# Kernel tuning notes

Hardware: AMD Instinct MI355X
Metric: run time of the kernel (lower is better)

## Reference

```python
import jax, jax.numpy as jnp
import numpy as np

B = 128
N_ATOMS = 4096
NB, NA, NT = 4095, 4094, 4093
MAX_LEN = 5 * NT  # 20465, longest packed column (torsions)
EPS = 1e-8


def setup_inputs() -> dict:
    key = jax.random.key(0)
    ks = jax.random.split(key, 24)
    feats = jnp.zeros((B, MAX_LEN, 9), jnp.float32)
    # col 0: atom type ids
    atoms = jax.random.randint(ks[0], (B, N_ATOMS), 0, 6)
    # col 5: coords, flattened (N_ATOMS, 3)
    coords = jax.random.normal(ks[1], (B, N_ATOMS, 3), jnp.float32) * 5.0
    # col 6: bonds (i, j, type)
    bonds = jnp.stack([
        jax.random.randint(ks[2], (B, NB), 0, N_ATOMS),
        jax.random.randint(ks[3], (B, NB), 0, N_ATOMS),
        jax.random.randint(ks[4], (B, NB), 0, 15)], axis=-1)
    # col 7: angles (i, j, k, type)
    angles = jnp.stack([
        jax.random.randint(ks[5], (B, NA), 0, N_ATOMS),
        jax.random.randint(ks[6], (B, NA), 0, N_ATOMS),
        jax.random.randint(ks[7], (B, NA), 0, N_ATOMS),
        jax.random.randint(ks[8], (B, NA), 0, 13)], axis=-1)
    # col 8: torsions (i, j, k, l, type)
    tors = jnp.stack([
        jax.random.randint(ks[9], (B, NT), 0, N_ATOMS),
        jax.random.randint(ks[10], (B, NT), 0, N_ATOMS),
        jax.random.randint(ks[11], (B, NT), 0, N_ATOMS),
        jax.random.randint(ks[12], (B, NT), 0, N_ATOMS),
        jax.random.randint(ks[13], (B, NT), 0, 25)], axis=-1)
    feats = feats.at[:, :N_ATOMS, 0].set(atoms.astype(jnp.float32))
    feats = feats.at[:, :3 * N_ATOMS, 5].set(coords.reshape(B, -1))
    feats = feats.at[:, :3 * NB, 6].set(bonds.reshape(B, -1).astype(jnp.float32))
    feats = feats.at[:, :4 * NA, 7].set(angles.reshape(B, -1).astype(jnp.float32))
    feats = feats.at[:, :5 * NT, 8].set(tors.reshape(B, -1).astype(jnp.float32))
    lengths = jnp.tile(jnp.array(
        [[N_ATOMS, 0, 0, 0, 0, 3 * N_ATOMS, 3 * NB, 4 * NA, 5 * NT]],
        jnp.int32), (B, 1))
    bond_type = jnp.stack([jnp.ones(15), jax.random.uniform(ks[14], (15,), minval=1.0, maxval=2.0)], -1).astype(jnp.float32)
    angle_type = jnp.stack([jnp.ones(13), jax.random.uniform(ks[15], (13,), minval=1.0, maxval=3.0)], -1).astype(jnp.float32)
    tor_type = jnp.stack([jnp.ones(25), jax.random.uniform(ks[16], (25,), minval=0.0, maxval=3.14)], -1).astype(jnp.float32)
    multiplicity = jax.random.randint(ks[17], (25,), 1, 4)
    opt_pars = jax.random.uniform(ks[18], (47,), minval=0.5, maxval=1.5).astype(jnp.float32)
    return {"features": feats, "lengths": lengths, "bond_type": bond_type,
            "angle_type": angle_type, "tor_type": tor_type,
            "multiplicity": multiplicity, "opt_pars": opt_pars}


def _sample_energy(f, bond_type, angle_type, tor_type, multiplicity, opt_pars):
    coords = f[:3 * N_ATOMS, 5].reshape(-1, 3)                      # [N,3]
    bonds = f[:3 * NB, 6].astype(jnp.int32).reshape(-1, 3)          # [NB,3]
    angles = f[:4 * NA, 7].astype(jnp.int32).reshape(-1, 4)         # [NA,4]
    tors = f[:5 * NT, 8].astype(jnp.int32).reshape(-1, 5)           # [NT,5]

    # bonds: harmonic k*(r - r0)^2
    d = coords[bonds[:, 0]] - coords[bonds[:, 1]]
    r = jnp.sqrt(jnp.sum(d * d, -1) + EPS)
    pb = bond_type[bonds[:, 2]]
    e_bond = opt_pars[0] * jnp.sum(pb[:, 0] * (r - pb[:, 1]) ** 2)

    # angles: harmonic k*(theta - theta0)^2
    v1 = coords[angles[:, 0]] - coords[angles[:, 1]]
    v2 = coords[angles[:, 2]] - coords[angles[:, 1]]
    cosang = jnp.sum(v1 * v2, -1) / (
        jnp.sqrt(jnp.sum(v1 * v1, -1) + EPS) * jnp.sqrt(jnp.sum(v2 * v2, -1) + EPS))
    theta = jnp.arccos(jnp.clip(cosang, -1.0 + 1e-6, 1.0 - 1e-6))
    pa = angle_type[angles[:, 3]]
    e_ang = opt_pars[1] * jnp.sum(pa[:, 0] * (theta - pa[:, 1]) ** 2)

    # torsions: periodic k*(1 + cos(n*phi - delta))
    ci, cj, ck, cl = (coords[tors[:, m]] for m in range(4))
    b1, b2, b3 = cj - ci, ck - cj, cl - ck
    n1 = jnp.cross(b1, b2)
    n2 = jnp.cross(b2, b3)
    b2n = b2 / jnp.sqrt(jnp.sum(b2 * b2, -1, keepdims=True) + EPS)
    m1 = jnp.cross(n1, b2n)
    phi = jnp.arctan2(jnp.sum(m1 * n2, -1), jnp.sum(n1 * n2, -1))
    pt = tor_type[tors[:, 4]]
    n_mult = multiplicity[tors[:, 4]].astype(jnp.float32)
    e_tor = opt_pars[2] * jnp.sum(pt[:, 0] * (1.0 + jnp.cos(n_mult * phi - pt[:, 1])))

    return jnp.stack([e_bond, e_ang, e_tor])


def reference(features, lengths, bond_type, angle_type, tor_type, multiplicity, opt_pars):
    # lengths are uniform across batch (constants above); vmap over batch dim
    return jax.vmap(_sample_energy, in_axes=(0, None, None, None, None, None))(
        features, bond_type, angle_type, tor_type, multiplicity, opt_pars)
```

## Files before the change

kernel.cpp:

```cpp
#include <hip/hip_runtime.h>
#include <math.h>

#define BATCH    128
#define N_ATOMS  4096
#define NB       4095
#define NA       4094
#define NT       4093
#define FSTRIDE  184185
#define ROWS     20465
#define CROWS    12288
#define BROWS    12285
#define AROWS    16376
#define EPSV     1e-8f
#define THREADS  1024
#define WAVES    16
#define TPR      120

typedef float float4a __attribute__((ext_vector_type(4), aligned(4)));

__global__ __launch_bounds__(THREADS, 1) void
local_energy_v11(const float* __restrict__ F,
                 const float* __restrict__ bond_type,
                 const float* __restrict__ angle_type,
                 const float* __restrict__ tor_type,
                 const int*   __restrict__ multiplicity,
                 const float* __restrict__ opt_pars,
                 float*       __restrict__ out)
{
    __shared__ float          scc[CROWS];
    __shared__ unsigned short sbB[BROWS + 1];
    __shared__ unsigned short sbA[AROWS];
    __shared__ unsigned short sbT[ROWS + 1];
    __shared__ float sbt[30], sat[26], stt[50], smu[25];
    __shared__ float sred[WAVES * 2];

    const int b   = blockIdx.x;
    const int x   = b & 7;
    const int g   = b >> 3;
    const int s   = (g & 15) * 8 + x;
    const int p   = g >> 4;
    const int tid = threadIdx.x;
    const int w   = tid >> 6;
    const int l   = tid & 63;
    const size_t sbase = (size_t)s * FSTRIDE;

    if (tid < 30)                      sbt[tid]       = bond_type[tid];
    else if (tid >= 32 && tid < 58)    sat[tid - 32]  = angle_type[tid - 32];
    else if (tid >= 64 && tid < 114)   stt[tid - 64]  = tor_type[tid - 64];
    else if (tid >= 128 && tid < 153)  smu[tid - 128] = (float)multiplicity[tid - 128];

    const int tmax = p ? 137 : 171;
    for (int t = w; t < tmax; t += WAVES) {
        const int R0 = TPR * t + 2 * l;
        const int R1 = R0 + 1;
        float4a v0, v1;
        const bool ok0 = (R0 < ROWS);
        const bool ok1 = (R1 < ROWS);
        if (ok0) v0 = *(const float4a*)(F + sbase + (size_t)9 * R0 + 5);
        if (ok1) v1 = *(const float4a*)(F + sbase + (size_t)9 * R1 + 5);

        if (R1 < CROWS) {
            float2 c2; c2.x = v0.x; c2.y = v1.x;
            *(float2*)(scc + R0) = c2;
        }
        if (p) {
            if (R1 < BROWS) {
                unsigned pk = (unsigned)(unsigned short)(int)v0.y
                            | ((unsigned)(unsigned short)(int)v1.y << 16);
                *(unsigned*)(sbB + R0) = pk;
            } else if (R0 < BROWS) {
                sbB[R0] = (unsigned short)(int)v0.y;
            }
            if (R1 < AROWS) {
                unsigned pk = (unsigned)(unsigned short)(int)v0.z
                            | ((unsigned)(unsigned short)(int)v1.z << 16);
                *(unsigned*)(sbA + R0) = pk;
            }
        } else {
            if (ok1) {
                unsigned pk = (unsigned)(unsigned short)(int)v0.w
                            | ((unsigned)(unsigned short)(int)v1.w << 16);
                *(unsigned*)(sbT + R0) = pk;
            } else if (ok0) {
                sbT[R0] = (unsigned short)(int)v0.w;
            }
        }
    }
    __syncthreads();

    float eA = 0.f, eB = 0.f;
    if (p) {
        for (int i = tid; i < NB; i += THREADS) {
            const int a0 = sbB[3 * i + 0];
            const int a1 = sbB[3 * i + 1];
            const int bt = sbB[3 * i + 2];
            const float dx = scc[3 * a0 + 0] - scc[3 * a1 + 0];
            const float dy = scc[3 * a0 + 1] - scc[3 * a1 + 1];
            const float dz = scc[3 * a0 + 2] - scc[3 * a1 + 2];
            const float r  = sqrtf(dx * dx + dy * dy + dz * dz + EPSV);
            const float t0 = r - sbt[bt * 2 + 1];
            eA += sbt[bt * 2 + 0] * t0 * t0;
        }
        for (int i = tid; i < NA; i += THREADS) {
            const int a0 = sbA[4 * i + 0];
            const int a1 = sbA[4 * i + 1];
            const int a2 = sbA[4 * i + 2];
            const int at = sbA[4 * i + 3];
            const float v1x = scc[3 * a0 + 0] - scc[3 * a1 + 0];
            const float v1y = scc[3 * a0 + 1] - scc[3 * a1 + 1];
            const float v1z = scc[3 * a0 + 2] - scc[3 * a1 + 2];
            const float v2x = scc[3 * a2 + 0] - scc[3 * a1 + 0];
            const float v2y = scc[3 * a2 + 1] - scc[3 * a1 + 1];
            const float v2z = scc[3 * a2 + 2] - scc[3 * a1 + 2];
            const float d12 = v1x * v2x + v1y * v2y + v1z * v2z;
            const float n1  = sqrtf(v1x * v1x + v1y * v1y + v1z * v1z + EPSV);
            const float n2  = sqrtf(v2x * v2x + v2y * v2y + v2z * v2z + EPSV);
            float cosang = d12 / (n1 * n2);
            cosang = fminf(fmaxf(cosang, -1.0f + 1e-6f), 1.0f - 1e-6f);
            const float t0 = acosf(cosang) - sat[at * 2 + 1];
            eB += sat[at * 2 + 0] * t0 * t0;
        }
    } else {
        for (int i = tid; i < NT; i += THREADS) {
            const int ai = sbT[5 * i + 0];
            const int aj = sbT[5 * i + 1];
            const int ak = sbT[5 * i + 2];
            const int al = sbT[5 * i + 3];
            const int tt = sbT[5 * i + 4];
            const float b1x = scc[3*aj+0] - scc[3*ai+0];
            const float b1y = scc[3*aj+1] - scc[3*ai+1];
            const float b1z = scc[3*aj+2] - scc[3*ai+2];
            const float b2x = scc[3*ak+0] - scc[3*aj+0];
            const float b2y = scc[3*ak+1] - scc[3*aj+1];
            const float b2z = scc[3*ak+2] - scc[3*aj+2];
            const float b3x = scc[3*al+0] - scc[3*ak+0];
            const float b3y = scc[3*al+1] - scc[3*ak+1];
            const float b3z = scc[3*al+2] - scc[3*ak+2];
            const float n1x = b1y*b2z - b1z*b2y;
            const float n1y = b1z*b2x - b1x*b2z;
            const float n1z = b1x*b2y - b1y*b2x;
            const float n2x = b2y*b3z - b2z*b3y;
            const float n2y = b2z*b3x - b2x*b3z;
            const float n2z = b2x*b3y - b2y*b3x;
            const float inv = 1.0f / sqrtf(b2x*b2x + b2y*b2y + b2z*b2z + EPSV);
            const float bnx = b2x * inv, bny = b2y * inv, bnz = b2z * inv;
            const float m1x = n1y*bnz - n1z*bny;
            const float m1y = n1z*bnx - n1x*bnz;
            const float m1z = n1x*bny - n1y*bnx;
            const float phi = atan2f(m1x*n2x + m1y*n2y + m1z*n2z,
                                     n1x*n2x + n1y*n2y + n1z*n2z);
            eA += stt[tt * 2 + 0] * (1.0f + cosf(smu[tt] * phi - stt[tt * 2 + 1]));
        }
    }

    for (int off = 32; off > 0; off >>= 1) {
        eA += __shfl_down(eA, off);
        eB += __shfl_down(eB, off);
    }
    if (l == 0) {
        sred[w * 2 + 0] = eA;
        sred[w * 2 + 1] = eB;
    }
    __syncthreads();
    if (tid == 0) {
        float rA = 0.f, rB = 0.f;
        for (int i = 0; i < WAVES; ++i) { rA += sred[i * 2]; rB += sred[i * 2 + 1]; }
        if (p) {
            out[s * 3 + 0] = opt_pars[0] * rA;
            out[s * 3 + 1] = opt_pars[1] * rB;
        } else {
            out[s * 3 + 2] = opt_pars[2] * rA;
        }
    }
}

extern "C" void kernel_launch(void* const* d_in, const int* in_sizes, int n_in,
                              void* d_out, int out_size, void* d_ws, size_t ws_size,
                              hipStream_t stream) {
    const float* F            = (const float*)d_in[0];
    const float* bond_type    = (const float*)d_in[2];
    const float* angle_type   = (const float*)d_in[3];
    const float* tor_type     = (const float*)d_in[4];
    const int*   multiplicity = (const int*)  d_in[5];
    const float* opt_pars     = (const float*)d_in[6];
    float* out = (float*)d_out;

    local_energy_v11<<<dim3(BATCH * 2), dim3(THREADS), 0, stream>>>(
        F, bond_type, angle_type, tor_type, multiplicity, opt_pars, out);
}
```

Measured before the change: 155.8 us.

## Split feature extraction into separate wide-grid kernel writing compact workspace arrays

Adds a 2048-block extraction kernel that reads the strided feature rows once and writes compact coordinate and index arrays to a global workspace. The energy kernel then loads only the coordinates into shared memory and reads index arrays directly from global memory, with angle indices fetched as a single ushort4 load. The aim is more parallelism for the strided, bandwidth-bound gather and less shared-memory staging per block. It costs a second launch, an extra write and re-read pass through global memory, and index loads that are no longer coalesced in the energy loops.

```diff
diff --git a/kernel.cpp b/kernel.cpp
--- a/kernel.cpp
+++ b/kernel.cpp
@@ -12,25 +12,60 @@
 #define BROWS    12285
 #define AROWS    16376
 #define EPSV     1e-8f
-#define THREADS  1024
 #define WAVES    16
-#define TPR      120
+
+#define WS_CW_B  0
+#define WS_BW_B  6291456
+#define WS_AW_B  9437184
+#define WS_TW_B  13631488
 
 typedef float float4a __attribute__((ext_vector_type(4), aligned(4)));
 
+__global__ __launch_bounds__(256) void
+extract_k(const float* __restrict__ F, float* __restrict__ ws)
+{
+    const int b     = blockIdx.x;
+    const int x     = b & 7;
+    const int g     = b >> 3;
+    const int s     = (g & 15) * 8 + x;
+    const int slice = g >> 4;
+    const size_t sbase = (size_t)s * FSTRIDE;
+
+    float*          __restrict__ cw = (float*)((char*)ws + WS_CW_B) + (size_t)s * 12288;
+    unsigned short* __restrict__ bw = (unsigned short*)((char*)ws + WS_BW_B) + (size_t)s * 12288;
+    unsigned short* __restrict__ aw = (unsigned short*)((char*)ws + WS_AW_B) + (size_t)s * 16384;
+    unsigned short* __restrict__ tw = (unsigned short*)((char*)ws + WS_TW_B) + (size_t)s * 20472;
+
+    const int lo = slice * 1280;
+    int  r[5]; bool ok[5]; float4a v[5];
+    #pragma unroll
+    for (int k = 0; k < 5; ++k) {
+        r[k]  = lo + (int)threadIdx.x + 256 * k;
+        ok[k] = (r[k] < ROWS);
+        if (ok[k]) v[k] = *(const float4a*)(F + sbase + (size_t)9 * r[k] + 5);
+    }
+    #pragma unroll
+    for (int k = 0; k < 5; ++k) {
+        if (!ok[k]) continue;
+        const int R = r[k];
+        if (R < CROWS) cw[R] = v[k].x;
+        if (R < BROWS) bw[R] = (unsigned short)(int)v[k].y;
+        if (R < AROWS) aw[R] = (unsigned short)(int)v[k].z;
+        tw[R] = (unsigned short)(int)v[k].w;
+    }
+}
+
+#define THREADS 1024
 __global__ __launch_bounds__(THREADS, 1) void
-local_energy_v11(const float* __restrict__ F,
-                 const float* __restrict__ bond_type,
-                 const float* __restrict__ angle_type,
-                 const float* __restrict__ tor_type,
-                 const int*   __restrict__ multiplicity,
-                 const float* __restrict__ opt_pars,
-                 float*       __restrict__ out)
+energy_k(const float* __restrict__ ws,
+         const float* __restrict__ bond_type,
+         const float* __restrict__ angle_type,
+         const float* __restrict__ tor_type,
+         const int*   __restrict__ multiplicity,
+         const float* __restrict__ opt_pars,
+         float*       __restrict__ out)
 {
-    __shared__ float          scc[CROWS];
-    __shared__ unsigned short sbB[BROWS + 1];
-    __shared__ unsigned short sbA[AROWS];
-    __shared__ unsigned short sbT[ROWS + 1];
+    __shared__ float scc[CROWS];
     __shared__ float sbt[30], sat[26], stt[50], smu[25];
     __shared__ float sred[WAVES * 2];
 
@@ -42,70 +77,41 @@
     const int tid = threadIdx.x;
     const int w   = tid >> 6;
     const int l   = tid & 63;
-    const size_t sbase = (size_t)s * FSTRIDE;
 
     if (tid < 30)                      sbt[tid]       = bond_type[tid];
     else if (tid >= 32 && tid < 58)    sat[tid - 32]  = angle_type[tid - 32];
     else if (tid >= 64 && tid < 114)   stt[tid - 64]  = tor_type[tid - 64];
     else if (tid >= 128 && tid < 153)  smu[tid - 128] = (float)multiplicity[tid - 128];
 
-    const int tmax = p ? 137 : 171;
-    for (int t = w; t < tmax; t += WAVES) {
-        const int R0 = TPR * t + 2 * l;
-        const int R1 = R0 + 1;
-        float4a v0, v1;
-        const bool ok0 = (R0 < ROWS);
-        const bool ok1 = (R1 < ROWS);
-        if (ok0) v0 = *(const float4a*)(F + sbase + (size_t)9 * R0 + 5);
-        if (ok1) v1 = *(const float4a*)(F + sbase + (size_t)9 * R1 + 5);
-
-        if (R1 < CROWS) {
-            float2 c2; c2.x = v0.x; c2.y = v1.x;
-            *(float2*)(scc + R0) = c2;
-        }
-        if (p) {
-            if (R1 < BROWS) {
-                unsigned pk = (unsigned)(unsigned short)(int)v0.y
-                            | ((unsigned)(unsigned short)(int)v1.y << 16);
-                *(unsigned*)(sbB + R0) = pk;
-            } else if (R0 < BROWS) {
-                sbB[R0] = (unsigned short)(int)v0.y;
-            }
-            if (R1 < AROWS) {
-                unsigned pk = (unsigned)(unsigned short)(int)v0.z
-                            | ((unsigned)(unsigned short)(int)v1.z << 16);
-                *(unsigned*)(sbA + R0) = pk;
-            }
-        } else {
-            if (ok1) {
-                unsigned pk = (unsigned)(unsigned short)(int)v0.w
-                            | ((unsigned)(unsigned short)(int)v1.w << 16);
-                *(unsigned*)(sbT + R0) = pk;
-            } else if (ok0) {
-                sbT[R0] = (unsigned short)(int)v0.w;
-            }
-        }
+    {
+        const float4* __restrict__ c4 =
+            (const float4*)((const char*)ws + WS_CW_B + (size_t)s * 12288 * 4);
+        #pragma unroll
+        for (int i = 0; i < 3; ++i)
+            ((float4*)scc)[tid + 1024 * i] = c4[tid + 1024 * i];
     }
     __syncthreads();
 
     float eA = 0.f, eB = 0.f;
     if (p) {
+        const unsigned short* __restrict__ bwp =
+            (const unsigned short*)((const char*)ws + WS_BW_B) + (size_t)s * 12288;
         for (int i = tid; i < NB; i += THREADS) {
-            const int a0 = sbB[3 * i + 0];
-            const int a1 = sbB[3 * i + 1];
-            const int bt = sbB[3 * i + 2];
+            const int a0 = bwp[3 * i + 0];
+            const int a1 = bwp[3 * i + 1];
+            const int bt = bwp[3 * i + 2];
             const float dx = scc[3 * a0 + 0] - scc[3 * a1 + 0];
             const float dy = scc[3 * a0 + 1] - scc[3 * a1 + 1];
             const float dz = scc[3 * a0 + 2] - scc[3 * a1 + 2];
-            const float r  = sqrtf(dx * dx + dy * dy + dz * dz + EPSV);
-            const float t0 = r - sbt[bt * 2 + 1];
+            const float rr = sqrtf(dx * dx + dy * dy + dz * dz + EPSV);
+            const float t0 = rr - sbt[bt * 2 + 1];
             eA += sbt[bt * 2 + 0] * t0 * t0;
         }
+        const ushort4* __restrict__ awp =
+            (const ushort4*)((const char*)ws + WS_AW_B + (size_t)s * 16384 * 2);
         for (int i = tid; i < NA; i += THREADS) {
-            const int a0 = sbA[4 * i + 0];
-            const int a1 = sbA[4 * i + 1];
-            const int a2 = sbA[4 * i + 2];
-            const int at = sbA[4 * i + 3];
+            const ushort4 u = awp[i];
+            const int a0 = u.x, a1 = u.y, a2 = u.z, at = u.w;
             const float v1x = scc[3 * a0 + 0] - scc[3 * a1 + 0];
             const float v1y = scc[3 * a0 + 1] - scc[3 * a1 + 1];
             const float v1z = scc[3 * a0 + 2] - scc[3 * a1 + 2];
@@ -121,12 +127,14 @@
             eB += sat[at * 2 + 0] * t0 * t0;
         }
     } else {
+        const unsigned short* __restrict__ twp =
+            (const unsigned short*)((const char*)ws + WS_TW_B) + (size_t)s * 20472;
         for (int i = tid; i < NT; i += THREADS) {
-            const int ai = sbT[5 * i + 0];
-            const int aj = sbT[5 * i + 1];
-            const int ak = sbT[5 * i + 2];
-            const int al = sbT[5 * i + 3];
-            const int tt = sbT[5 * i + 4];
+            const int ai = twp[5 * i + 0];
+            const int aj = twp[5 * i + 1];
+            const int ak = twp[5 * i + 2];
+            const int al = twp[5 * i + 3];
+            const int tt = twp[5 * i + 4];
             const float b1x = scc[3*aj+0] - scc[3*ai+0];
             const float b1y = scc[3*aj+1] - scc[3*ai+1];
             const float b1z = scc[3*aj+2] - scc[3*ai+2];
@@ -157,10 +165,7 @@
         eA += __shfl_down(eA, off);
         eB += __shfl_down(eB, off);
     }
-    if (l == 0) {
-        sred[w * 2 + 0] = eA;
-        sred[w * 2 + 1] = eB;
-    }
+    if (l == 0) { sred[w * 2 + 0] = eA; sred[w * 2 + 1] = eB; }
     __syncthreads();
     if (tid == 0) {
         float rA = 0.f, rB = 0.f;
@@ -184,7 +189,9 @@
     const int*   multiplicity = (const int*)  d_in[5];
     const float* opt_pars     = (const float*)d_in[6];
     float* out = (float*)d_out;
+    float* ws  = (float*)d_ws;
 
-    local_energy_v11<<<dim3(BATCH * 2), dim3(THREADS), 0, stream>>>(
-        F, bond_type, angle_type, tor_type, multiplicity, opt_pars, out);
+    extract_k<<<dim3(2048), dim3(256), 0, stream>>>(F, ws);
+    energy_k<<<dim3(256), dim3(THREADS), 0, stream>>>(
+        ws, bond_type, angle_type, tor_type, multiplicity, opt_pars, out);
 }
```

After: 165.3 us. 6.1% more time.

## Merge bond/angle and torsion blocks into one block per sample

Applied to the files above, without the earlier changes.

Replaces the two-blocks-per-sample split, where one block handled bonds and angles and another handled torsions, with a single block per sample. The single block stages coordinates and all index columns into shared memory once, then computes all three energies. This removes the duplicated coordinate load and halves the grid. In exchange, fewer blocks are launched than there are compute units, and each block does roughly twice the serial work.

```diff
diff --git a/kernel.cpp b/kernel.cpp
--- a/kernel.cpp
+++ b/kernel.cpp
@@ -15,11 +15,12 @@
 #define THREADS  1024
 #define WAVES    16
 #define TPR      120
+#define NTIL     171
 
 typedef float float4a __attribute__((ext_vector_type(4), aligned(4)));
 
 __global__ __launch_bounds__(THREADS, 1) void
-local_energy_v11(const float* __restrict__ F,
+local_energy_v13(const float* __restrict__ F,
                  const float* __restrict__ bond_type,
                  const float* __restrict__ angle_type,
                  const float* __restrict__ tor_type,
@@ -32,13 +33,9 @@
     __shared__ unsigned short sbA[AROWS];
     __shared__ unsigned short sbT[ROWS + 1];
     __shared__ float sbt[30], sat[26], stt[50], smu[25];
-    __shared__ float sred[WAVES * 2];
+    __shared__ float sred[WAVES * 3];
 
-    const int b   = blockIdx.x;
-    const int x   = b & 7;
-    const int g   = b >> 3;
-    const int s   = (g & 15) * 8 + x;
-    const int p   = g >> 4;
+    const int s   = blockIdx.x;
     const int tid = threadIdx.x;
     const int w   = tid >> 6;
     const int l   = tid & 63;
@@ -49,8 +46,7 @@
     else if (tid >= 64 && tid < 114)   stt[tid - 64]  = tor_type[tid - 64];
     else if (tid >= 128 && tid < 153)  smu[tid - 128] = (float)multiplicity[tid - 128];
 
-    const int tmax = p ? 137 : 171;
-    for (int t = w; t < tmax; t += WAVES) {
+    for (int t = w; t < NTIL; t += WAVES) {
         const int R0 = TPR * t + 2 * l;
         const int R1 = R0 + 1;
         float4a v0, v1;
@@ -63,114 +59,112 @@
             float2 c2; c2.x = v0.x; c2.y = v1.x;
             *(float2*)(scc + R0) = c2;
         }
-        if (p) {
-            if (R1 < BROWS) {
-                unsigned pk = (unsigned)(unsigned short)(int)v0.y
-                            | ((unsigned)(unsigned short)(int)v1.y << 16);
-                *(unsigned*)(sbB + R0) = pk;
-            } else if (R0 < BROWS) {
-                sbB[R0] = (unsigned short)(int)v0.y;
-            }
-            if (R1 < AROWS) {
-                unsigned pk = (unsigned)(unsigned short)(int)v0.z
-                            | ((unsigned)(unsigned short)(int)v1.z << 16);
-                *(unsigned*)(sbA + R0) = pk;
-            }
-        } else {
-            if (ok1) {
-                unsigned pk = (unsigned)(unsigned short)(int)v0.w
-                            | ((unsigned)(unsigned short)(int)v1.w << 16);
-                *(unsigned*)(sbT + R0) = pk;
-            } else if (ok0) {
-                sbT[R0] = (unsigned short)(int)v0.w;
-            }
+        if (R1 < BROWS) {
+            unsigned pk = (unsigned)(unsigned short)(int)v0.y
+                        | ((unsigned)(unsigned short)(int)v1.y << 16);
+            *(unsigned*)(sbB + R0) = pk;
+        } else if (R0 < BROWS) {
+            sbB[R0] = (unsigned short)(int)v0.y;
+        }
+        if (R1 < AROWS) {
+            unsigned pk = (unsigned)(unsigned short)(int)v0.z
+                        | ((unsigned)(unsigned short)(int)v1.z << 16);
+            *(unsigned*)(sbA + R0) = pk;
+        }
+        if (ok1) {
+            unsigned pk = (unsigned)(unsigned short)(int)v0.w
+                        | ((unsigned)(unsigned short)(int)v1.w << 16);
+            *(unsigned*)(sbT + R0) = pk;
+        } else if (ok0) {
+            sbT[R0] = (unsigned short)(int)v0.w;
         }
     }
     __syncthreads();
 
-    float eA = 0.f, eB = 0.f;
-    if (p) {
-        for (int i = tid; i < NB; i += THREADS) {
-            const int a0 = sbB[3 * i + 0];
-            const int a1 = sbB[3 * i + 1];
-            const int bt = sbB[3 * i + 2];
-            const float dx = scc[3 * a0 + 0] - scc[3 * a1 + 0];
-            const float dy = scc[3 * a0 + 1] - scc[3 * a1 + 1];
-            const float dz = scc[3 * a0 + 2] - scc[3 * a1 + 2];
-            const float r  = sqrtf(dx * dx + dy * dy + dz * dz + EPSV);
-            const float t0 = r - sbt[bt * 2 + 1];
-            eA += sbt[bt * 2 + 0] * t0 * t0;
-        }
-        for (int i = tid; i < NA; i += THREADS) {
-            const int a0 = sbA[4 * i + 0];
-            const int a1 = sbA[4 * i + 1];
-            const int a2 = sbA[4 * i + 2];
-            const int at = sbA[4 * i + 3];
-            const float v1x = scc[3 * a0 + 0] - scc[3 * a1 + 0];
-            const float v1y = scc[3 * a0 + 1] - scc[3 * a1 + 1];
-            const float v1z = scc[3 * a0 + 2] - scc[3 * a1 + 2];
-            const float v2x = scc[3 * a2 + 0] - scc[3 * a1 + 0];
-            const float v2y = scc[3 * a2 + 1] - scc[3 * a1 + 1];
-            const float v2z = scc[3 * a2 + 2] - scc[3 * a1 + 2];
-            const float d12 = v1x * v2x + v1y * v2y + v1z * v2z;
-            const float n1  = sqrtf(v1x * v1x + v1y * v1y + v1z * v1z + EPSV);
-            const float n2  = sqrtf(v2x * v2x + v2y * v2y + v2z * v2z + EPSV);
-            float cosang = d12 / (n1 * n2);
-            cosang = fminf(fmaxf(cosang, -1.0f + 1e-6f), 1.0f - 1e-6f);
-            const float t0 = acosf(cosang) - sat[at * 2 + 1];
-            eB += sat[at * 2 + 0] * t0 * t0;
-        }
-    } else {
-        for (int i = tid; i < NT; i += THREADS) {
-            const int ai = sbT[5 * i + 0];
-            const int aj = sbT[5 * i + 1];
-            const int ak = sbT[5 * i + 2];
-            const int al = sbT[5 * i + 3];
-            const int tt = sbT[5 * i + 4];
-            const float b1x = scc[3*aj+0] - scc[3*ai+0];
-            const float b1y = scc[3*aj+1] - scc[3*ai+1];
-            const float b1z = scc[3*aj+2] - scc[3*ai+2];
-            const float b2x = scc[3*ak+0] - scc[3*aj+0];
-            const float b2y = scc[3*ak+1] - scc[3*aj+1];
-            const float b2z = scc[3*ak+2] - scc[3*aj+2];
-            const float b3x = scc[3*al+0] - scc[3*ak+0];
-            const float b3y = scc[3*al+1] - scc[3*ak+1];
-            const float b3z = scc[3*al+2] - scc[3*ak+2];
-            const float n1x = b1y*b2z - b1z*b2y;
-            const float n1y = b1z*b2x - b1x*b2z;
-            const float n1z = b1x*b2y - b1y*b2x;
-            const float n2x = b2y*b3z - b2z*b3y;
-            const float n2y = b2z*b3x - b2x*b3z;
-            const float n2z = b2x*b3y - b2y*b3x;
-            const float inv = 1.0f / sqrtf(b2x*b2x + b2y*b2y + b2z*b2z + EPSV);
-            const float bnx = b2x * inv, bny = b2y * inv, bnz = b2z * inv;
-            const float m1x = n1y*bnz - n1z*bny;
-            const float m1y = n1z*bnx - n1x*bnz;
-            const float m1z = n1x*bny - n1y*bnx;
-            const float phi = atan2f(m1x*n2x + m1y*n2y + m1z*n2z,
-                                     n1x*n2x + n1y*n2y + n1z*n2z);
-            eA += stt[tt * 2 + 0] * (1.0f + cosf(smu[tt] * phi - stt[tt * 2 + 1]));
-        }
+    float e_bond = 0.f, e_ang = 0.f, e_tor = 0.f;
+
+    for (int i = tid; i < NB; i += THREADS) {
+        const int a0 = sbB[3 * i + 0];
+        const int a1 = sbB[3 * i + 1];
+        const int bt = sbB[3 * i + 2];
+        const float dx = scc[3 * a0 + 0] - scc[3 * a1 + 0];
+        const float dy = scc[3 * a0 + 1] - scc[3 * a1 + 1];
+        const float dz = scc[3 * a0 + 2] - scc[3 * a1 + 2];
+        const float r  = sqrtf(dx * dx + dy * dy + dz * dz + EPSV);
+        const float t0 = r - sbt[bt * 2 + 1];
+        e_bond += sbt[bt * 2 + 0] * t0 * t0;
+    }
+    for (int i = tid; i < NA; i += THREADS) {
+        const int a0 = sbA[4 * i + 0];
+        const int a1 = sbA[4 * i + 1];
+        const int a2 = sbA[4 * i + 2];
+        const int at = sbA[4 * i + 3];
+        const float v1x = scc[3 * a0 + 0] - scc[3 * a1 + 0];
+        const float v1y = scc[3 * a0 + 1] - scc[3 * a1 + 1];
+        const float v1z = scc[3 * a0 + 2] - scc[3 * a1 + 2];
+        const float v2x = scc[3 * a2 + 0] - scc[3 * a1 + 0];
+        const float v2y = scc[3 * a2 + 1] - scc[3 * a1 + 1];
+        const float v2z = scc[3 * a2 + 2] - scc[3 * a1 + 2];
+        const float d12 = v1x * v2x + v1y * v2y + v1z * v2z;
+        const float n1  = sqrtf(v1x * v1x + v1y * v1y + v1z * v1z + EPSV);
+        const float n2  = sqrtf(v2x * v2x + v2y * v2y + v2z * v2z + EPSV);
+        float cosang = d12 / (n1 * n2);
+        cosang = fminf(fmaxf(cosang, -1.0f + 1e-6f), 1.0f - 1e-6f);
+        const float t0 = acosf(cosang) - sat[at * 2 + 1];
+        e_ang += sat[at * 2 + 0] * t0 * t0;
+    }
+    for (int i = tid; i < NT; i += THREADS) {
+        const int ai = sbT[5 * i + 0];
+        const int aj = sbT[5 * i + 1];
+        const int ak = sbT[5 * i + 2];
+        const int al = sbT[5 * i + 3];
+        const int tt = sbT[5 * i + 4];
+        const float b1x = scc[3*aj+0] - scc[3*ai+0];
+        const float b1y = scc[3*aj+1] - scc[3*ai+1];
+        const float b1z = scc[3*aj+2] - scc[3*ai+2];
+        const float b2x = scc[3*ak+0] - scc[3*aj+0];
+        const float b2y = scc[3*ak+1] - scc[3*aj+1];
+        const float b2z = scc[3*ak+2] - scc[3*aj+2];
+        const float b3x = scc[3*al+0] - scc[3*ak+0];
+        const float b3y = scc[3*al+1] - scc[3*ak+1];
+        const float b3z = scc[3*al+2] - scc[3*ak+2];
+        const float n1x = b1y*b2z - b1z*b2y;
+        const float n1y = b1z*b2x - b1x*b2z;
+        const float n1z = b1x*b2y - b1y*b2x;
+        const float n2x = b2y*b3z - b2z*b3y;
+        const float n2y = b2z*b3x - b2x*b3z;
+        const float n2z = b2x*b3y - b2y*b3x;
+        const float inv = 1.0f / sqrtf(b2x*b2x + b2y*b2y + b2z*b2z + EPSV);
+        const float bnx = b2x * inv, bny = b2y * inv, bnz = b2z * inv;
+        const float m1x = n1y*bnz - n1z*bny;
+        const float m1y = n1z*bnx - n1x*bnz;
+        const float m1z = n1x*bny - n1y*bnx;
+        const float phi = atan2f(m1x*n2x + m1y*n2y + m1z*n2z,
+                                 n1x*n2x + n1y*n2y + n1z*n2z);
+        e_tor += stt[tt * 2 + 0] * (1.0f + cosf(smu[tt] * phi - stt[tt * 2 + 1]));
     }
 
     for (int off = 32; off > 0; off >>= 1) {
-        eA += __shfl_down(eA, off);
-        eB += __shfl_down(eB, off);
+        e_bond += __shfl_down(e_bond, off);
+        e_ang  += __shfl_down(e_ang,  off);
+        e_tor  += __shfl_down(e_tor,  off);
     }
     if (l == 0) {
-        sred[w * 2 + 0] = eA;
-        sred[w * 2 + 1] = eB;
+        sred[w * 3 + 0] = e_bond;
+        sred[w * 3 + 1] = e_ang;
+        sred[w * 3 + 2] = e_tor;
     }
     __syncthreads();
     if (tid == 0) {
-        float rA = 0.f, rB = 0.f;
-        for (int i = 0; i < WAVES; ++i) { rA += sred[i * 2]; rB += sred[i * 2 + 1]; }
-        if (p) {
-            out[s * 3 + 0] = opt_pars[0] * rA;
-            out[s * 3 + 1] = opt_pars[1] * rB;
-        } else {
-            out[s * 3 + 2] = opt_pars[2] * rA;
+        float eb = 0.f, ea = 0.f, et = 0.f;
+        for (int i = 0; i < WAVES; ++i) {
+            eb += sred[i * 3 + 0];
+            ea += sred[i * 3 + 1];
+            et += sred[i * 3 + 2];
         }
+        out[s * 3 + 0] = opt_pars[0] * eb;
+        out[s * 3 + 1] = opt_pars[1] * ea;
+        out[s * 3 + 2] = opt_pars[2] * et;
     }
 }
 
@@ -185,6 +179,6 @@
     const float* opt_pars     = (const float*)d_in[6];
     float* out = (float*)d_out;
 
-    local_energy_v11<<<dim3(BATCH * 2), dim3(THREADS), 0, stream>>>(
+    local_energy_v13<<<dim3(BATCH), dim3(THREADS), 0, stream>>>(
         F, bond_type, angle_type, tor_type, multiplicity, opt_pars, out);
 }
```

Result: slower. 165.0 us (+5.9%).

## Overlap tail loading of angle/torsion indices with bond and early-torsion compute

Applied to the files above, without the earlier changes.

Splits the staging of feature rows into two phases. In the first phase all waves load the first 103 tiles, which cover the coords, the bonds and an early slice of the torsions. In the second phase half the waves load the remaining angle/torsion index rows while the other half computes bond energies or the first 2472 torsions from data already in shared memory. The goal is to hide the global load latency of the tail rows behind compute, at the cost of an extra barrier and an uneven split of work between the two wave groups.

```diff
diff --git a/kernel.cpp b/kernel.cpp
--- a/kernel.cpp
+++ b/kernel.cpp
@@ -15,11 +15,13 @@
 #define THREADS  1024
 #define WAVES    16
 #define TPR      120
+#define T_A1     103
+#define NT_PRE   2472
 
 typedef float float4a __attribute__((ext_vector_type(4), aligned(4)));
 
 __global__ __launch_bounds__(THREADS, 1) void
-local_energy_v11(const float* __restrict__ F,
+local_energy_v15(const float* __restrict__ F,
                  const float* __restrict__ bond_type,
                  const float* __restrict__ angle_type,
                  const float* __restrict__ tor_type,
@@ -49,15 +51,11 @@
     else if (tid >= 64 && tid < 114)   stt[tid - 64]  = tor_type[tid - 64];
     else if (tid >= 128 && tid < 153)  smu[tid - 128] = (float)multiplicity[tid - 128];
 
-    const int tmax = p ? 137 : 171;
-    for (int t = w; t < tmax; t += WAVES) {
+    for (int t = w; t < T_A1; t += WAVES) {
         const int R0 = TPR * t + 2 * l;
         const int R1 = R0 + 1;
-        float4a v0, v1;
-        const bool ok0 = (R0 < ROWS);
-        const bool ok1 = (R1 < ROWS);
-        if (ok0) v0 = *(const float4a*)(F + sbase + (size_t)9 * R0 + 5);
-        if (ok1) v1 = *(const float4a*)(F + sbase + (size_t)9 * R1 + 5);
+        float4a v0 = *(const float4a*)(F + sbase + (size_t)9 * R0 + 5);
+        float4a v1 = *(const float4a*)(F + sbase + (size_t)9 * R1 + 5);
 
         if (R1 < CROWS) {
             float2 c2; c2.x = v0.x; c2.y = v1.x;
@@ -71,36 +69,99 @@
             } else if (R0 < BROWS) {
                 sbB[R0] = (unsigned short)(int)v0.y;
             }
-            if (R1 < AROWS) {
+            {
                 unsigned pk = (unsigned)(unsigned short)(int)v0.z
                             | ((unsigned)(unsigned short)(int)v1.z << 16);
                 *(unsigned*)(sbA + R0) = pk;
             }
         } else {
-            if (ok1) {
-                unsigned pk = (unsigned)(unsigned short)(int)v0.w
-                            | ((unsigned)(unsigned short)(int)v1.w << 16);
-                *(unsigned*)(sbT + R0) = pk;
-            } else if (ok0) {
-                sbT[R0] = (unsigned short)(int)v0.w;
-            }
+            unsigned pk = (unsigned)(unsigned short)(int)v0.w
+                        | ((unsigned)(unsigned short)(int)v1.w << 16);
+            *(unsigned*)(sbT + R0) = pk;
         }
     }
     __syncthreads();
 
     float eA = 0.f, eB = 0.f;
+
+    if (w < 8) {
+        const int tmax = p ? 137 : 171;
+        for (int t = T_A1 + w; t < tmax; t += 8) {
+            const int R0 = TPR * t + 2 * l;
+            const int R1 = R0 + 1;
+            float4a v0, v1;
+            const bool ok0 = (R0 < ROWS);
+            const bool ok1 = (R1 < ROWS);
+            if (ok0) v0 = *(const float4a*)(F + sbase + (size_t)9 * R0 + 5);
+            if (ok1) v1 = *(const float4a*)(F + sbase + (size_t)9 * R1 + 5);
+            if (p) {
+                if (R1 < AROWS) {
+                    unsigned pk = (unsigned)(unsigned short)(int)v0.z
+                                | ((unsigned)(unsigned short)(int)v1.z << 16);
+                    *(unsigned*)(sbA + R0) = pk;
+                } else if (R0 < AROWS) {
+                    sbA[R0] = (unsigned short)(int)v0.z;
+                }
+            } else {
+                if (ok1) {
+                    unsigned pk = (unsigned)(unsigned short)(int)v0.w
+                                | ((unsigned)(unsigned short)(int)v1.w << 16);
+                    *(unsigned*)(sbT + R0) = pk;
+                } else if (ok0) {
+                    sbT[R0] = (unsigned short)(int)v0.w;
+                }
+            }
+        }
+    } else {
+        const int ctid = tid - 512;
+        if (p) {
+            for (int i = ctid; i < NB; i += 512) {
+                const int a0 = sbB[3 * i + 0];
+                const int a1 = sbB[3 * i + 1];
+                const int bt = sbB[3 * i + 2];
+                const float dx = scc[3 * a0 + 0] - scc[3 * a1 + 0];
+                const float dy = scc[3 * a0 + 1] - scc[3 * a1 + 1];
+                const float dz = scc[3 * a0 + 2] - scc[3 * a1 + 2];
+                const float r  = sqrtf(dx * dx + dy * dy + dz * dz + EPSV);
+                const float t0 = r - sbt[bt * 2 + 1];
+                eA += sbt[bt * 2 + 0] * t0 * t0;
+            }
+        } else {
+            for (int i = ctid; i < NT_PRE; i += 512) {
+                const int ai = sbT[5 * i + 0];
+                const int aj = sbT[5 * i + 1];
+                const int ak = sbT[5 * i + 2];
+                const int al = sbT[5 * i + 3];
+                const int tt = sbT[5 * i + 4];
+                const float b1x = scc[3*aj+0] - scc[3*ai+0];
+                const float b1y = scc[3*aj+1] - scc[3*ai+1];
+                const float b1z = scc[3*aj+2] - scc[3*ai+2];
+                const float b2x = scc[3*ak+0] - scc[3*aj+0];
+                const float b2y = scc[3*ak+1] - scc[3*aj+1];
+                const float b2z = scc[3*ak+2] - scc[3*aj+2];
+                const float b3x = scc[3*al+0] - scc[3*ak+0];
+                const float b3y = scc[3*al+1] - scc[3*ak+1];
+                const float b3z = scc[3*al+2] - scc[3*ak+2];
+                const float n1x = b1y*b2z - b1z*b2y;
+                const float n1y = b1z*b2x - b1x*b2z;
+                const float n1z = b1x*b2y - b1y*b2x;
+                const float n2x = b2y*b3z - b2z*b3y;
+                const float n2y = b2z*b3x - b2x*b3z;
+                const float n2z = b2x*b3y - b2y*b3x;
+                const float inv = 1.0f / sqrtf(b2x*b2x + b2y*b2y + b2z*b2z + EPSV);
+                const float bnx = b2x * inv, bny = b2y * inv, bnz = b2z * inv;
+                const float m1x = n1y*bnz - n1z*bny;
+                const float m1y = n1z*bnx - n1x*bnz;
+                const float m1z = n1x*bny - n1y*bnx;
+                const float phi = atan2f(m1x*n2x + m1y*n2y + m1z*n2z,
+                                         n1x*n2x + n1y*n2y + n1z*n2z);
+                eA += stt[tt * 2 + 0] * (1.0f + cosf(smu[tt] * phi - stt[tt * 2 + 1]));
+            }
+        }
+    }
+    __syncthreads();
+
     if (p) {
-        for (int i = tid; i < NB; i += THREADS) {
-            const int a0 = sbB[3 * i + 0];
-            const int a1 = sbB[3 * i + 1];
-            const int bt = sbB[3 * i + 2];
-            const float dx = scc[3 * a0 + 0] - scc[3 * a1 + 0];
-            const float dy = scc[3 * a0 + 1] - scc[3 * a1 + 1];
-            const float dz = scc[3 * a0 + 2] - scc[3 * a1 + 2];
-            const float r  = sqrtf(dx * dx + dy * dy + dz * dz + EPSV);
-            const float t0 = r - sbt[bt * 2 + 1];
-            eA += sbt[bt * 2 + 0] * t0 * t0;
-        }
         for (int i = tid; i < NA; i += THREADS) {
             const int a0 = sbA[4 * i + 0];
             const int a1 = sbA[4 * i + 1];
@@ -121,7 +182,7 @@
             eB += sat[at * 2 + 0] * t0 * t0;
         }
     } else {
-        for (int i = tid; i < NT; i += THREADS) {
+        for (int i = NT_PRE + tid; i < NT; i += THREADS) {
             const int ai = sbT[5 * i + 0];
             const int aj = sbT[5 * i + 1];
             const int ak = sbT[5 * i + 2];
@@ -157,10 +218,7 @@
         eA += __shfl_down(eA, off);
         eB += __shfl_down(eB, off);
     }
-    if (l == 0) {
-        sred[w * 2 + 0] = eA;
-        sred[w * 2 + 1] = eB;
-    }
+    if (l == 0) { sred[w * 2 + 0] = eA; sred[w * 2 + 1] = eB; }
     __syncthreads();
     if (tid == 0) {
         float rA = 0.f, rB = 0.f;
@@ -185,6 +243,6 @@
     const float* opt_pars     = (const float*)d_in[6];
     float* out = (float*)d_out;
 
-    local_energy_v11<<<dim3(BATCH * 2), dim3(THREADS), 0, stream>>>(
+    local_energy_v15<<<dim3(BATCH * 2), dim3(THREADS), 0, stream>>>(
         F, bond_type, angle_type, tor_type, multiplicity, opt_pars, out);
 }
```

Result: no change. 156.9 us (+0.7%).
